# Kernel optimization log

Measured on AMD Instinct MI355X. Metric: run time of the kernel, lower is better.

The kernel has to match this reference:

```python
import jax, jax.numpy as jnp
import numpy as np

B, N, F, H, C, HID = 2, 2048, 64, 4, 32, 128
HIN = H * C  # 128, GAT output width (concat heads)


def setup_inputs() -> dict:
    key = jax.random.key(0)
    ks = jax.random.split(key, 16)
    glorot = jax.nn.initializers.glorot_normal()
    x = jax.random.normal(ks[0], (B, N, F), jnp.float32)
    a = (jax.random.uniform(ks[1], (B, N, N)) < 0.01).astype(jnp.float32)
    a = jnp.maximum(a, jnp.eye(N, dtype=jnp.float32)[None])
    h = jax.random.normal(ks[2], (B, N, HID), jnp.float32)
    # GATConv params (spektral batch mode, concat_heads=True)
    kernel = glorot(ks[3], (F, H, C), jnp.float32)
    attn_self = glorot(ks[4], (H, C), jnp.float32)
    attn_nei = glorot(ks[5], (H, C), jnp.float32)
    bias_gat = jnp.zeros((HIN,), jnp.float32)
    # GRU-style gate params
    b_u = glorot(ks[6], (N, 1), jnp.float32)
    b_r = glorot(ks[7], (N, 1), jnp.float32)
    b_c = glorot(ks[8], (N, 1), jnp.float32)
    W_u = glorot(ks[9], (HID + HIN, HID), jnp.float32)
    W_r = glorot(ks[10], (HID + HIN, HID), jnp.float32)
    W_c = glorot(ks[11], (HID + HIN, HID), jnp.float32)
    # bilinear decoder (p) weight
    R_p = glorot(ks[12], (HID, HID), jnp.float32)
    return {"x": x, "a": a, "h": h, "kernel": kernel, "attn_self": attn_self,
            "attn_nei": attn_nei, "bias_gat": bias_gat, "b_u": b_u, "b_r": b_r,
            "b_c": b_c, "W_u": W_u, "W_r": W_r, "W_c": W_c, "R_p": R_p}


def _gat(x, a, kernel, attn_self, attn_nei, bias_gat):
    # x: [B,N,F] -> per-head features xp: [B,N,H,C]
    xp = jnp.einsum('bnf,fhc->bnhc', x, kernel)
    es = jnp.einsum('bnhc,hc->bnh', xp, attn_self)   # target score
    en = jnp.einsum('bnhc,hc->bnh', xp, attn_nei)    # source score
    # e[b,i,j,h] = leakyrelu(es_i + en_j), masked by adjacency
    e = jax.nn.leaky_relu(es[:, :, None, :] + en[:, None, :, :], 0.2)
    e = e + (-1e9) * (1.0 - a)[..., None]
    alpha = jax.nn.softmax(e, axis=2)                # softmax over sources j
    out = jnp.einsum('bijh,bjhc->bihc', alpha, xp)   # aggregate
    return out.reshape(out.shape[0], out.shape[1], -1) + bias_gat  # [B,N,H*C]


def reference(x, a, h, kernel, attn_self, attn_nei, bias_gat,
              b_u, b_r, b_c, W_u, W_r, W_c, R_p):
    conv_u = _gat(x, a, kernel, attn_self, attn_nei, bias_gat)  # [B,N,HIN]
    z = jnp.concatenate([conv_u, h], axis=-1)                    # [B,N,HIN+HID]
    u = jax.nn.sigmoid(b_u + z @ W_u)                            # b_u [N,1] broadcasts
    r = jax.nn.sigmoid(b_r + z @ W_r)
    zc = jnp.concatenate([conv_u, r * h], axis=-1)
    c = jnp.tanh(b_c + zc @ W_c)
    h_prime = u * h + (1.0 - u) * c                              # [B,N,HID]
    A = jnp.einsum('bnh,hk,bmk->bnm', h_prime, R_p, h_prime)     # bilinear decode [B,N,N]
    return A, h_prime
```

## Files before the change

kernel.cpp:

```cpp
#include <hip/hip_runtime.h>
#include <hip/hip_bf16.h>
#include <math.h>

#define NB 2
#define NN 2048
#define FD 64
#define NH 4
#define HIDD 128
#define ROWS_TOT (NB*NN)

#define XP_OFF   0
#define ES_OFF   524288
#define EN_OFF   540672
#define CU_OFF   557056
#define TBF_OFF  1081344
#define HPBF_OFF 1343488
#define WUH_OFF  1605632
#define WUL_OFF  1622016
#define WRH_OFF  1638400
#define WRL_OFF  1654784
#define WCH_OFF  1671168
#define WCL_OFF  1687552
#define RPH_OFF  1703936
#define RPL_OFF  1712128

#define A_ELEMS (NB*NN*NN)

typedef __attribute__((ext_vector_type(8))) short bf16x8;
typedef __attribute__((ext_vector_type(8))) unsigned short ushort8;
typedef __attribute__((ext_vector_type(4))) unsigned short ushort4v;
typedef __attribute__((ext_vector_type(4))) float f32x4;

#define MFMA_BF16(a,b,c) __builtin_amdgcn_mfma_f32_16x16x32_bf16((a),(b),(c),0,0,0)

static __device__ inline unsigned short f2bf(float x) {
  __hip_bfloat16 b = __float2bfloat16(x);
  unsigned short u; __builtin_memcpy(&u, &b, 2); return u;
}
static __device__ inline float bf2f(unsigned short u) {
  __hip_bfloat16 b; __builtin_memcpy(&b, &u, 2); return __bfloat162float(b);
}
static __device__ inline void split2(float x, unsigned short& hi, unsigned short& lo) {
  hi = f2bf(x);
  lo = f2bf(x - bf2f(hi));
}

__global__ __launch_bounds__(256) void k0_prep(
    const float* __restrict__ Wu, const float* __restrict__ Wr,
    const float* __restrict__ Wc, const float* __restrict__ Rp,
    unsigned short* __restrict__ wuh, unsigned short* __restrict__ wul,
    unsigned short* __restrict__ wrh, unsigned short* __restrict__ wrl,
    unsigned short* __restrict__ wch, unsigned short* __restrict__ wcl,
    unsigned short* __restrict__ rph, unsigned short* __restrict__ rpl)
{
  const int gid = blockIdx.x*256 + threadIdx.x;
  if (gid < 98304) {
    const int which = gid >> 15;
    const int loc = gid & 32767;
    const int j = loc >> 8, k = loc & 255;
    const float* W = which == 0 ? Wu : (which == 1 ? Wr : Wc);
    unsigned short* oh = which == 0 ? wuh : (which == 1 ? wrh : wch);
    unsigned short* ol = which == 0 ? wul : (which == 1 ? wrl : wcl);
    unsigned short h, l; split2(W[k*128 + j], h, l);
    oh[loc] = h; ol[loc] = l;
  } else if (gid < 114688) {
    const int loc = gid - 98304;
    const int j = loc >> 7, k = loc & 127;
    unsigned short h, l; split2(Rp[k*128 + j], h, l);
    rph[loc] = h; rpl[loc] = l;
  }
}

__global__ __launch_bounds__(256) void k1_xp(
    const float* __restrict__ x, const float* __restrict__ kern,
    const float* __restrict__ as_, const float* __restrict__ an_,
    float* __restrict__ xp, float* __restrict__ es, float* __restrict__ en)
{
  __shared__ float xr[8][FD];
  const int t = threadIdx.x;
  const int row0 = blockIdx.x * 8;
  for (int idx = t; idx < 8*FD; idx += 256)
    xr[idx >> 6][idx & 63] = x[(size_t)row0*FD + idx];
  __syncthreads();
  const int c4 = (t & 31) * 4;
  const int rq = t >> 5;
  const float4 asv = *(const float4*)(as_ + c4);
  const float4 anv = *(const float4*)(an_ + c4);
  float4 acc = make_float4(0.f, 0.f, 0.f, 0.f);
  for (int f = 0; f < FD; ++f) {
    const float4 kv = *(const float4*)(kern + f*128 + c4);
    const float xv = xr[rq][f];
    acc.x = fmaf(xv, kv.x, acc.x);
    acc.y = fmaf(xv, kv.y, acc.y);
    acc.z = fmaf(xv, kv.z, acc.z);
    acc.w = fmaf(xv, kv.w, acc.w);
  }
  const int grow = row0 + rq;
  *(float4*)(xp + (size_t)grow*128 + c4) = acc;
  float s  = acc.x*asv.x + acc.y*asv.y + acc.z*asv.z + acc.w*asv.w;
  float n_ = acc.x*anv.x + acc.y*anv.y + acc.z*anv.z + acc.w*anv.w;
#pragma unroll
  for (int mk = 4; mk >= 1; mk >>= 1) {
    s  += __shfl_xor(s,  mk, 64);
    n_ += __shfl_xor(n_, mk, 64);
  }
  if ((t & 7) == 0) {
    const int h = (t & 31) >> 3;
    es[grow*NH + h] = s; en[grow*NH + h] = n_;
  }
}

__global__ __launch_bounds__(256) void k2_attn(
    const float* __restrict__ a, const float* __restrict__ xp,
    const float* __restrict__ es, const float* __restrict__ en,
    const float* __restrict__ bias, float* __restrict__ cu)
{
  __shared__ unsigned short sidx[4][NN];
  __shared__ float swl[4][64][NH];
  const int t = threadIdx.x;
  const int ln = t & 63, wv = t >> 6;
  const int row = blockIdx.x * 4 + wv;
  const int b = row >> 11;
  const float4 esi = *(const float4*)(es + (size_t)row*NH);

  int deg = 0;
  const float4* arow4 = (const float4*)(a + (size_t)row*NN);
#pragma unroll
  for (int cch = 0; cch < 8; ++cch) {
    const float4 v = arow4[cch*64 + ln];
    const int j0 = cch*256 + ln*4;
    const float vv[4] = {v.x, v.y, v.z, v.w};
#pragma unroll
    for (int q = 0; q < 4; ++q) {
      const unsigned long long m = __ballot(vv[q] > 0.5f);
      if (vv[q] > 0.5f) {
        const int pos = deg + (int)__popcll(m & ((1ull << ln) - 1ull));
        sidx[wv][pos] = (unsigned short)(j0 + q);
      }
      deg += (int)__popcll(m);
    }
  }

  const int col0 = ln, col1 = ln + 64;
  const int h0 = ln >> 5;
  float m0=-1e30f, m1=-1e30f, m2=-1e30f, m3=-1e30f;
  float s0=0.f, s1=0.f, s2=0.f, s3=0.f;
  float acc0=0.f, acc1=0.f;
  for (int base = 0; base < deg; base += 64) {
    const int rem = min(64, deg - base);
    float t0=-1e30f, t1=-1e30f, t2=-1e30f, t3=-1e30f;
    if (ln < rem) {
      const int j = sidx[wv][base + ln];
      const float4 e4 = *(const float4*)(en + (size_t)(b*NN + j)*NH);
      t0 = esi.x + e4.x; t0 = t0 > 0.f ? t0 : 0.2f*t0;
      t1 = esi.y + e4.y; t1 = t1 > 0.f ? t1 : 0.2f*t1;
      t2 = esi.z + e4.z; t2 = t2 > 0.f ? t2 : 0.2f*t2;
      t3 = esi.w + e4.w; t3 = t3 > 0.f ? t3 : 0.2f*t3;
    }
    float c0=t0, c1=t1, c2=t2, c3=t3;
#pragma unroll
    for (int mk = 32; mk >= 1; mk >>= 1) {
      c0 = fmaxf(c0, __shfl_xor(c0, mk));
      c1 = fmaxf(c1, __shfl_xor(c1, mk));
      c2 = fmaxf(c2, __shfl_xor(c2, mk));
      c3 = fmaxf(c3, __shfl_xor(c3, mk));
    }
    const float nm0 = fmaxf(m0,c0), nm1 = fmaxf(m1,c1);
    const float nm2 = fmaxf(m2,c2), nm3 = fmaxf(m3,c3);
    const float r0 = expf(m0-nm0), r1 = expf(m1-nm1);
    const float r2 = expf(m2-nm2), r3 = expf(m3-nm3);
    s0 *= r0; s1 *= r1; s2 *= r2; s3 *= r3;
    float w0=0.f, w1=0.f, w2=0.f, w3=0.f;
    if (ln < rem) {
      w0 = expf(t0-nm0); w1 = expf(t1-nm1);
      w2 = expf(t2-nm2); w3 = expf(t3-nm3);
    }
    float u0=w0, u1=w1, u2=w2, u3=w3;
#pragma unroll
    for (int mk = 32; mk >= 1; mk >>= 1) {
      u0 += __shfl_xor(u0, mk);
      u1 += __shfl_xor(u1, mk);
      u2 += __shfl_xor(u2, mk);
      u3 += __shfl_xor(u3, mk);
    }
    s0 += u0; s1 += u1; s2 += u2; s3 += u3;
    acc0 *= (h0 ? r1 : r0);
    acc1 *= (h0 ? r3 : r2);
    swl[wv][ln][0] = w0; swl[wv][ln][1] = w1;
    swl[wv][ln][2] = w2; swl[wv][ln][3] = w3;
#pragma unroll 4
    for (int k = 0; k < rem; ++k) {
      const int j = sidx[wv][base + k];
      const float* xr = xp + (size_t)(b*NN + j)*128;
      acc0 = fmaf(swl[wv][k][h0],     xr[col0], acc0);
      acc1 = fmaf(swl[wv][k][2 + h0], xr[col1], acc1);
    }
    m0=nm0; m1=nm1; m2=nm2; m3=nm3;
  }
  const float den0 = h0 ? s1 : s0;
  const float den1 = h0 ? s3 : s2;
  cu[(size_t)row*128 + col0] = acc0/den0 + bias[col0];
  cu[(size_t)row*128 + col1] = acc1/den1 + bias[col1];
}

__global__ __launch_bounds__(256) void k3_mfma(
    const float* __restrict__ cu_, const float* __restrict__ hin,
    const float* __restrict__ bu, const float* __restrict__ br,
    const float* __restrict__ bc,
    const unsigned short* __restrict__ wuh, const unsigned short* __restrict__ wul,
    const unsigned short* __restrict__ wrh, const unsigned short* __restrict__ wrl,
    const unsigned short* __restrict__ wch, const unsigned short* __restrict__ wcl,
    const unsigned short* __restrict__ rph, const unsigned short* __restrict__ rpl,
    float* __restrict__ hp_out,
    __hip_bfloat16* __restrict__ hp_bf, __hip_bfloat16* __restrict__ t_bf)
{
  __shared__ __align__(16) char zH[16*512];
  __shared__ __align__(16) char zL[16*512];
  __shared__ __align__(16) char rhH[16*256];
  __shared__ __align__(16) char rhL[16*256];
  __shared__ __align__(16) char hpH[16*256];
  __shared__ __align__(16) char hpLo[16*256];
  const int t = threadIdx.x;
  const int row0 = blockIdx.x * 16;

#pragma unroll
  for (int i = 0; i < 4; ++i) {
    const int q = t + 256*i;
    const int r = q >> 6;
    const int c = (q & 63) * 4;
    float4 v;
    if (c < 128) v = *(const float4*)(cu_ + (size_t)(row0+r)*128 + c);
    else         v = *(const float4*)(hin + (size_t)(row0+r)*128 + (c-128));
    unsigned short hx, lx, hy, ly, hz, lz, hw, lw;
    split2(v.x, hx, lx); split2(v.y, hy, ly);
    split2(v.z, hz, lz); split2(v.w, hw, lw);
    ushort4v h4; h4[0]=hx; h4[1]=hy; h4[2]=hz; h4[3]=hw;
    ushort4v l4; l4[0]=lx; l4[1]=ly; l4[2]=lz; l4[3]=lw;
    const int byte = (c*2) ^ ((r & 7) << 4);
    *(ushort4v*)(zH + r*512 + byte) = h4;
    *(ushort4v*)(zL + r*512 + byte) = l4;
  }
  __syncthreads();

  const int ln = t & 63, wv = t >> 6;
  const int n0 = wv * 32;
  const int lr = ln & 15, kid = ln >> 4;
  const int sw = (lr & 7) << 4;
  const f32x4 zero = {0.f, 0.f, 0.f, 0.f};

  f32x4 accU[2] = {zero, zero}, accR[2] = {zero, zero};
#pragma unroll
  for (int ks = 0; ks < 8; ++ks) {
    const int kb = ks*64 + kid*16;
    const bf16x8 ah = *(const bf16x8*)(zH + lr*512 + (kb ^ sw));
    const bf16x8 al = *(const bf16x8*)(zL + lr*512 + (kb ^ sw));
#pragma unroll
    for (int nt = 0; nt < 2; ++nt) {
      const int j = n0 + nt*16 + lr;
      const bf16x8 buH = *(const bf16x8*)((const char*)wuh + j*512 + kb);
      const bf16x8 buL = *(const bf16x8*)((const char*)wul + j*512 + kb);
      const bf16x8 brH = *(const bf16x8*)((const char*)wrh + j*512 + kb);
      const bf16x8 brL = *(const bf16x8*)((const char*)wrl + j*512 + kb);
      accU[nt] = MFMA_BF16(ah, buH, accU[nt]);
      accU[nt] = MFMA_BF16(ah, buL, accU[nt]);
      accU[nt] = MFMA_BF16(al, buH, accU[nt]);
      accR[nt] = MFMA_BF16(ah, brH, accR[nt]);
      accR[nt] = MFMA_BF16(ah, brL, accR[nt]);
      accR[nt] = MFMA_BF16(al, brH, accR[nt]);
    }
  }

  float hval[2][4], uval[2][4];
#pragma unroll
  for (int nt = 0; nt < 2; ++nt) {
    const int colg = n0 + nt*16 + lr;
#pragma unroll
    for (int reg = 0; reg < 4; ++reg) {
      const int row16 = kid*4 + reg;
      const int grow = row0 + row16;
      const int nrow = grow & (NN-1);
      const float h_ = hin[(size_t)grow*128 + colg];
      const float uv = 1.f/(1.f + expf(-(bu[nrow] + accU[nt][reg])));
      const float rv = 1.f/(1.f + expf(-(br[nrow] + accR[nt][reg])));
      hval[nt][reg] = h_; uval[nt][reg] = uv;
      unsigned short hs, ls; split2(rv * h_, hs, ls);
      const int byte = (colg*2) ^ ((row16 & 7) << 4);
      *(unsigned short*)(rhH + row16*256 + byte) = hs;
      *(unsigned short*)(rhL + row16*256 + byte) = ls;
    }
  }
  __syncthreads();

  f32x4 accC[2] = {zero, zero};
#pragma unroll
  for (int ks = 0; ks < 8; ++ks) {
    const int kb = ks*64 + kid*16;
    bf16x8 ah, al;
    if (ks < 4) {
      ah = *(const bf16x8*)(zH + lr*512 + (kb ^ sw));
      al = *(const bf16x8*)(zL + lr*512 + (kb ^ sw));
    } else {
      const int kb2 = (ks-4)*64 + kid*16;
      ah = *(const bf16x8*)(rhH + lr*256 + (kb2 ^ sw));
      al = *(const bf16x8*)(rhL + lr*256 + (kb2 ^ sw));
    }
#pragma unroll
    for (int nt = 0; nt < 2; ++nt) {
      const int j = n0 + nt*16 + lr;
      const bf16x8 bH = *(const bf16x8*)((const char*)wch + j*512 + kb);
      const bf16x8 bL = *(const bf16x8*)((const char*)wcl + j*512 + kb);
      accC[nt] = MFMA_BF16(ah, bH, accC[nt]);
      accC[nt] = MFMA_BF16(ah, bL, accC[nt]);
      accC[nt] = MFMA_BF16(al, bH, accC[nt]);
    }
  }

#pragma unroll
  for (int nt = 0; nt < 2; ++nt) {
    const int colg = n0 + nt*16 + lr;
#pragma unroll
    for (int reg = 0; reg < 4; ++reg) {
      const int row16 = kid*4 + reg;
      const int grow = row0 + row16;
      const int nrow = grow & (NN-1);
      const float cc = tanhf(bc[nrow] + accC[nt][reg]);
      const float uv = uval[nt][reg];
      const float hpv = uv*hval[nt][reg] + (1.f - uv)*cc;
      hp_out[(size_t)grow*128 + colg] = hpv;
      hp_bf[(size_t)grow*128 + colg] = __float2bfloat16(hpv);
      unsigned short hs, ls; split2(hpv, hs, ls);
      const int byte = (colg*2) ^ ((row16 & 7) << 4);
      *(unsigned short*)(hpH  + row16*256 + byte) = hs;
      *(unsigned short*)(hpLo + row16*256 + byte) = ls;
    }
  }
  __syncthreads();

  f32x4 accT[2] = {zero, zero};
#pragma unroll
  for (int ks = 0; ks < 4; ++ks) {
    const int kb = ks*64 + kid*16;
    const bf16x8 ah = *(const bf16x8*)(hpH  + lr*256 + (kb ^ sw));
    const bf16x8 al = *(const bf16x8*)(hpLo + lr*256 + (kb ^ sw));
#pragma unroll
    for (int nt = 0; nt < 2; ++nt) {
      const int j = n0 + nt*16 + lr;
      const bf16x8 bH = *(const bf16x8*)((const char*)rph + j*256 + kb);
      const bf16x8 bL = *(const bf16x8*)((const char*)rpl + j*256 + kb);
      accT[nt] = MFMA_BF16(ah, bH, accT[nt]);
      accT[nt] = MFMA_BF16(ah, bL, accT[nt]);
      accT[nt] = MFMA_BF16(al, bH, accT[nt]);
    }
  }
#pragma unroll
  for (int nt = 0; nt < 2; ++nt) {
    const int colg = n0 + nt*16 + lr;
#pragma unroll
    for (int reg = 0; reg < 4; ++reg) {
      const int grow = row0 + kid*4 + reg;
      t_bf[(size_t)grow*128 + colg] = __float2bfloat16(accT[nt][reg]);
    }
  }
}

__global__ __launch_bounds__(256) void k4b_dec(
    const __hip_bfloat16* __restrict__ t_bf,
    const __hip_bfloat16* __restrict__ hp_bf,
    float* __restrict__ A)
{
  __shared__ __align__(16) char Alds[128*256];
  __shared__ __align__(16) char Blds[128*256];
  const int t = threadIdx.x;
  const int ln = t & 63, wv = t >> 6;
  const int b = blockIdx.z;
  const int i0 = blockIdx.y * 128, j0 = blockIdx.x * 128;

  {
    const int sub = ln >> 4;
    const int cb  = (ln & 15) * 16;
#pragma unroll
    for (int q = 0; q < 8; ++q) {
      const int chunk = wv*8 + q;
      const int row = chunk*4 + sub;
      const int scb = cb ^ ((row & 7) << 4);
      const ushort8 va = *(const ushort8*)
          ((const char*)(t_bf + ((size_t)(b*NN) + i0 + row)*128) + cb);
      *(ushort8*)(Alds + row*256 + scb) = va;
      const ushort8 vb = *(const ushort8*)
          ((const char*)(hp_bf + ((size_t)(b*NN) + j0 + row)*128) + cb);
      *(ushort8*)(Blds + row*256 + scb) = vb;
    }
  }
  __syncthreads();

  const int wr = wv >> 1, wc = wv & 1;
  const int lrow = ln & 15;
  const int kid  = ln >> 4;
  f32x4 acc[4][4];
  const f32x4 zero = {0.f, 0.f, 0.f, 0.f};
#pragma unroll
  for (int m = 0; m < 4; ++m)
#pragma unroll
    for (int n = 0; n < 4; ++n) acc[m][n] = zero;

#pragma unroll
  for (int ks = 0; ks < 4; ++ks) {
    const int kb = ks*64 + kid*16;
    bf16x8 af[4], bfr[4];
#pragma unroll
    for (int m = 0; m < 4; ++m) {
      const int arow = wr*64 + m*16 + lrow;
      af[m] = *(const bf16x8*)(Alds + arow*256 + (kb ^ ((arow & 7) << 4)));
      const int brow = wc*64 + m*16 + lrow;
      bfr[m] = *(const bf16x8*)(Blds + brow*256 + (kb ^ ((brow & 7) << 4)));
    }
#pragma unroll
    for (int m = 0; m < 4; ++m)
#pragma unroll
      for (int n = 0; n < 4; ++n)
        acc[m][n] = MFMA_BF16(af[m], bfr[n], acc[m][n]);
  }

#pragma unroll
  for (int m = 0; m < 4; ++m) {
    const int grow = i0 + wr*64 + m*16 + (ln >> 4)*4;
#pragma unroll
    for (int n = 0; n < 4; ++n) {
      const int gcol = j0 + wc*64 + n*16 + (ln & 15);
      float* Ap = A + ((size_t)b*NN + grow)*NN + gcol;
#pragma unroll
      for (int r = 0; r < 4; ++r)
        Ap[(size_t)r*NN] = acc[m][n][r];
    }
  }
}

extern "C" void kernel_launch(void* const* d_in, const int* in_sizes, int n_in,
                              void* d_out, int out_size, void* d_ws, size_t ws_size,
                              hipStream_t stream)
{
  const float* x    = (const float*)d_in[0];
  const float* a    = (const float*)d_in[1];
  const float* h    = (const float*)d_in[2];
  const float* kern = (const float*)d_in[3];
  const float* as_  = (const float*)d_in[4];
  const float* an_  = (const float*)d_in[5];
  const float* bias = (const float*)d_in[6];
  const float* bu   = (const float*)d_in[7];
  const float* br   = (const float*)d_in[8];
  const float* bc   = (const float*)d_in[9];
  const float* Wu   = (const float*)d_in[10];
  const float* Wr   = (const float*)d_in[11];
  const float* Wc   = (const float*)d_in[12];
  const float* Rp   = (const float*)d_in[13];
  (void)in_sizes; (void)n_in; (void)out_size; (void)ws_size;

  float* ws = (float*)d_ws;
  float* xp = ws + XP_OFF;
  float* es = ws + ES_OFF;
  float* en = ws + EN_OFF;
  float* cu = ws + CU_OFF;
  __hip_bfloat16* t_bf  = (__hip_bfloat16*)(ws + TBF_OFF);
  __hip_bfloat16* hp_bf = (__hip_bfloat16*)(ws + HPBF_OFF);
  unsigned short* wuh = (unsigned short*)(ws + WUH_OFF);
  unsigned short* wul = (unsigned short*)(ws + WUL_OFF);
  unsigned short* wrh = (unsigned short*)(ws + WRH_OFF);
  unsigned short* wrl = (unsigned short*)(ws + WRL_OFF);
  unsigned short* wch = (unsigned short*)(ws + WCH_OFF);
  unsigned short* wcl = (unsigned short*)(ws + WCL_OFF);
  unsigned short* rph = (unsigned short*)(ws + RPH_OFF);
  unsigned short* rpl = (unsigned short*)(ws + RPL_OFF);

  float* A  = (float*)d_out;
  float* hp = (float*)d_out + A_ELEMS;

  hipLaunchKernelGGL(k0_prep, dim3(448), dim3(256), 0, stream,
                     Wu, Wr, Wc, Rp, wuh, wul, wrh, wrl, wch, wcl, rph, rpl);
  hipLaunchKernelGGL(k1_xp,   dim3(ROWS_TOT/8), dim3(256), 0, stream,
                     x, kern, as_, an_, xp, es, en);
  hipLaunchKernelGGL(k2_attn, dim3(ROWS_TOT/4), dim3(256), 0, stream,
                     a, xp, es, en, bias, cu);
  hipLaunchKernelGGL(k3_mfma, dim3(ROWS_TOT/16), dim3(256), 0, stream,
                     cu, h, bu, br, bc, wuh, wul, wrh, wrl, wch, wcl, rph, rpl,
                     hp, hp_bf, t_bf);
  hipLaunchKernelGGL(k4b_dec, dim3(NN/128, NN/128, NB), dim3(256), 0, stream,
                     t_bf, hp_bf, A);
}
```

Baseline: 153.3 us.

## Pre-swizzle weights into MFMA fragment order, widen GRU block, stage decoder output

The prep kernel now stores split bf16 weights in per-lane MFMA fragment order, so the gate kernel reads B operands as fully coalesced 16-byte vectors. The gate kernel is widened to 512 threads, with each wave owning one 16-column tile instead of two. The decoder kernel stages its 128x128 fp32 tile through padded LDS (reusing the A/B buffers) and writes rows as coalesced float4, replacing scattered 4-byte stores. This costs an extra LDS round trip and two barriers in the decoder, plus more LDS per block, which may reduce occupancy.

```diff
diff --git a/kernel.cpp b/kernel.cpp
--- a/kernel.cpp
+++ b/kernel.cpp
@@ -57,7 +57,12 @@
   if (gid < 98304) {
     const int which = gid >> 15;
     const int loc = gid & 32767;
-    const int j = loc >> 8, k = loc & 255;
+    const int e  = loc & 7;
+    const int ln = (loc >> 3) & 63;
+    const int ks = (loc >> 9) & 7;
+    const int jt = loc >> 12;
+    const int j = jt*16 + (ln & 15);
+    const int k = ks*32 + ((ln >> 4) << 3) + e;
     const float* W = which == 0 ? Wu : (which == 1 ? Wr : Wc);
     unsigned short* oh = which == 0 ? wuh : (which == 1 ? wrh : wch);
     unsigned short* ol = which == 0 ? wul : (which == 1 ? wrl : wcl);
@@ -65,7 +70,12 @@
     oh[loc] = h; ol[loc] = l;
   } else if (gid < 114688) {
     const int loc = gid - 98304;
-    const int j = loc >> 7, k = loc & 127;
+    const int e  = loc & 7;
+    const int ln = (loc >> 3) & 63;
+    const int ks = (loc >> 9) & 3;
+    const int jt = loc >> 11;
+    const int j = jt*16 + (ln & 15);
+    const int k = ks*32 + ((ln >> 4) << 3) + e;
     unsigned short h, l; split2(Rp[k*128 + j], h, l);
     rph[loc] = h; rpl[loc] = l;
   }
@@ -203,7 +213,7 @@
   cu[(size_t)row*128 + col1] = acc1/den1 + bias[col1];
 }
 
-__global__ __launch_bounds__(256) void k3_mfma(
+__global__ __launch_bounds__(512) void k3_mfma(
     const float* __restrict__ cu_, const float* __restrict__ hin,
     const float* __restrict__ bu, const float* __restrict__ br,
     const float* __restrict__ bc,
@@ -224,8 +234,8 @@
   const int row0 = blockIdx.x * 16;
 
 #pragma unroll
-  for (int i = 0; i < 4; ++i) {
-    const int q = t + 256*i;
+  for (int i = 0; i < 2; ++i) {
+    const int q = t + 512*i;
     const int r = q >> 6;
     const int c = (q & 63) * 4;
     float4 v;
@@ -243,55 +253,56 @@
   __syncthreads();
 
   const int ln = t & 63, wv = t >> 6;
-  const int n0 = wv * 32;
   const int lr = ln & 15, kid = ln >> 4;
   const int sw = (lr & 7) << 4;
+  const int colg = wv*16 + lr;
   const f32x4 zero = {0.f, 0.f, 0.f, 0.f};
-
-  f32x4 accU[2] = {zero, zero}, accR[2] = {zero, zero};
+  const bf16x8* wuhF = (const bf16x8*)wuh;
+  const bf16x8* wulF = (const bf16x8*)wul;
+  const bf16x8* wrhF = (const bf16x8*)wrh;
+  const bf16x8* wrlF = (const bf16x8*)wrl;
+  const bf16x8* wchF = (const bf16x8*)wch;
+  const bf16x8* wclF = (const bf16x8*)wcl;
+  const bf16x8* rphF = (const bf16x8*)rph;
+  const bf16x8* rplF = (const bf16x8*)rpl;
+
+  f32x4 accU = zero, accR = zero;
 #pragma unroll
   for (int ks = 0; ks < 8; ++ks) {
     const int kb = ks*64 + kid*16;
     const bf16x8 ah = *(const bf16x8*)(zH + lr*512 + (kb ^ sw));
     const bf16x8 al = *(const bf16x8*)(zL + lr*512 + (kb ^ sw));
-#pragma unroll
-    for (int nt = 0; nt < 2; ++nt) {
-      const int j = n0 + nt*16 + lr;
-      const bf16x8 buH = *(const bf16x8*)((const char*)wuh + j*512 + kb);
-      const bf16x8 buL = *(const bf16x8*)((const char*)wul + j*512 + kb);
-      const bf16x8 brH = *(const bf16x8*)((const char*)wrh + j*512 + kb);
-      const bf16x8 brL = *(const bf16x8*)((const char*)wrl + j*512 + kb);
-      accU[nt] = MFMA_BF16(ah, buH, accU[nt]);
-      accU[nt] = MFMA_BF16(ah, buL, accU[nt]);
-      accU[nt] = MFMA_BF16(al, buH, accU[nt]);
-      accR[nt] = MFMA_BF16(ah, brH, accR[nt]);
-      accR[nt] = MFMA_BF16(ah, brL, accR[nt]);
-      accR[nt] = MFMA_BF16(al, brH, accR[nt]);
-    }
-  }
-
-  float hval[2][4], uval[2][4];
-#pragma unroll
-  for (int nt = 0; nt < 2; ++nt) {
-    const int colg = n0 + nt*16 + lr;
-#pragma unroll
-    for (int reg = 0; reg < 4; ++reg) {
-      const int row16 = kid*4 + reg;
-      const int grow = row0 + row16;
-      const int nrow = grow & (NN-1);
-      const float h_ = hin[(size_t)grow*128 + colg];
-      const float uv = 1.f/(1.f + expf(-(bu[nrow] + accU[nt][reg])));
-      const float rv = 1.f/(1.f + expf(-(br[nrow] + accR[nt][reg])));
-      hval[nt][reg] = h_; uval[nt][reg] = uv;
-      unsigned short hs, ls; split2(rv * h_, hs, ls);
-      const int byte = (colg*2) ^ ((row16 & 7) << 4);
-      *(unsigned short*)(rhH + row16*256 + byte) = hs;
-      *(unsigned short*)(rhL + row16*256 + byte) = ls;
-    }
-  }
-  __syncthreads();
-
-  f32x4 accC[2] = {zero, zero};
+    const int fb = (wv*8 + ks)*64 + ln;
+    const bf16x8 buH = wuhF[fb];
+    const bf16x8 buL = wulF[fb];
+    const bf16x8 brH = wrhF[fb];
+    const bf16x8 brL = wrlF[fb];
+    accU = MFMA_BF16(ah, buH, accU);
+    accU = MFMA_BF16(ah, buL, accU);
+    accU = MFMA_BF16(al, buH, accU);
+    accR = MFMA_BF16(ah, brH, accR);
+    accR = MFMA_BF16(ah, brL, accR);
+    accR = MFMA_BF16(al, brH, accR);
+  }
+
+  float hval[4], uval[4];
+#pragma unroll
+  for (int reg = 0; reg < 4; ++reg) {
+    const int row16 = kid*4 + reg;
+    const int grow = row0 + row16;
+    const int nrow = grow & (NN-1);
+    const float h_ = hin[(size_t)grow*128 + colg];
+    const float uv = 1.f/(1.f + expf(-(bu[nrow] + accU[reg])));
+    const float rv = 1.f/(1.f + expf(-(br[nrow] + accR[reg])));
+    hval[reg] = h_; uval[reg] = uv;
+    unsigned short hs, ls; split2(rv * h_, hs, ls);
+    const int byte = (colg*2) ^ ((row16 & 7) << 4);
+    *(unsigned short*)(rhH + row16*256 + byte) = hs;
+    *(unsigned short*)(rhL + row16*256 + byte) = ls;
+  }
+  __syncthreads();
+
+  f32x4 accC = zero;
 #pragma unroll
   for (int ks = 0; ks < 8; ++ks) {
     const int kb = ks*64 + kid*16;
@@ -304,62 +315,48 @@
       ah = *(const bf16x8*)(rhH + lr*256 + (kb2 ^ sw));
       al = *(const bf16x8*)(rhL + lr*256 + (kb2 ^ sw));
     }
-#pragma unroll
-    for (int nt = 0; nt < 2; ++nt) {
-      const int j = n0 + nt*16 + lr;
-      const bf16x8 bH = *(const bf16x8*)((const char*)wch + j*512 + kb);
-      const bf16x8 bL = *(const bf16x8*)((const char*)wcl + j*512 + kb);
-      accC[nt] = MFMA_BF16(ah, bH, accC[nt]);
-      accC[nt] = MFMA_BF16(ah, bL, accC[nt]);
-      accC[nt] = MFMA_BF16(al, bH, accC[nt]);
-    }
-  }
-
-#pragma unroll
-  for (int nt = 0; nt < 2; ++nt) {
-    const int colg = n0 + nt*16 + lr;
-#pragma unroll
-    for (int reg = 0; reg < 4; ++reg) {
-      const int row16 = kid*4 + reg;
-      const int grow = row0 + row16;
-      const int nrow = grow & (NN-1);
-      const float cc = tanhf(bc[nrow] + accC[nt][reg]);
-      const float uv = uval[nt][reg];
-      const float hpv = uv*hval[nt][reg] + (1.f - uv)*cc;
-      hp_out[(size_t)grow*128 + colg] = hpv;
-      hp_bf[(size_t)grow*128 + colg] = __float2bfloat16(hpv);
-      unsigned short hs, ls; split2(hpv, hs, ls);
-      const int byte = (colg*2) ^ ((row16 & 7) << 4);
-      *(unsigned short*)(hpH  + row16*256 + byte) = hs;
-      *(unsigned short*)(hpLo + row16*256 + byte) = ls;
-    }
-  }
-  __syncthreads();
-
-  f32x4 accT[2] = {zero, zero};
+    const int fb = (wv*8 + ks)*64 + ln;
+    const bf16x8 bH = wchF[fb];
+    const bf16x8 bL = wclF[fb];
+    accC = MFMA_BF16(ah, bH, accC);
+    accC = MFMA_BF16(ah, bL, accC);
+    accC = MFMA_BF16(al, bH, accC);
+  }
+
+#pragma unroll
+  for (int reg = 0; reg < 4; ++reg) {
+    const int row16 = kid*4 + reg;
+    const int grow = row0 + row16;
+    const int nrow = grow & (NN-1);
+    const float cc = tanhf(bc[nrow] + accC[reg]);
+    const float uv = uval[reg];
+    const float hpv = uv*hval[reg] + (1.f - uv)*cc;
+    hp_out[(size_t)grow*128 + colg] = hpv;
+    hp_bf[(size_t)grow*128 + colg] = __float2bfloat16(hpv);
+    unsigned short hs, ls; split2(hpv, hs, ls);
+    const int byte = (colg*2) ^ ((row16 & 7) << 4);
+    *(unsigned short*)(hpH  + row16*256 + byte) = hs;
+    *(unsigned short*)(hpLo + row16*256 + byte) = ls;
+  }
+  __syncthreads();
+
+  f32x4 accT = zero;
 #pragma unroll
   for (int ks = 0; ks < 4; ++ks) {
     const int kb = ks*64 + kid*16;
     const bf16x8 ah = *(const bf16x8*)(hpH  + lr*256 + (kb ^ sw));
     const bf16x8 al = *(const bf16x8*)(hpLo + lr*256 + (kb ^ sw));
-#pragma unroll
-    for (int nt = 0; nt < 2; ++nt) {
-      const int j = n0 + nt*16 + lr;
-      const bf16x8 bH = *(const bf16x8*)((const char*)rph + j*256 + kb);
-      const bf16x8 bL = *(const bf16x8*)((const char*)rpl + j*256 + kb);
-      accT[nt] = MFMA_BF16(ah, bH, accT[nt]);
-      accT[nt] = MFMA_BF16(ah, bL, accT[nt]);
-      accT[nt] = MFMA_BF16(al, bH, accT[nt]);
-    }
-  }
-#pragma unroll
-  for (int nt = 0; nt < 2; ++nt) {
-    const int colg = n0 + nt*16 + lr;
-#pragma unroll
-    for (int reg = 0; reg < 4; ++reg) {
-      const int grow = row0 + kid*4 + reg;
-      t_bf[(size_t)grow*128 + colg] = __float2bfloat16(accT[nt][reg]);
-    }
+    const int fb = (wv*4 + ks)*64 + ln;
+    const bf16x8 bH = rphF[fb];
+    const bf16x8 bL = rplF[fb];
+    accT = MFMA_BF16(ah, bH, accT);
+    accT = MFMA_BF16(ah, bL, accT);
+    accT = MFMA_BF16(al, bH, accT);
+  }
+#pragma unroll
+  for (int reg = 0; reg < 4; ++reg) {
+    const int grow = row0 + kid*4 + reg;
+    t_bf[(size_t)grow*128 + colg] = __float2bfloat16(accT[reg]);
   }
 }
 
@@ -368,8 +365,10 @@
     const __hip_bfloat16* __restrict__ hp_bf,
     float* __restrict__ A)
 {
-  __shared__ __align__(16) char Alds[128*256];
-  __shared__ __align__(16) char Blds[128*256];
+  __shared__ __align__(16) char smem[128*132*4];
+  char* Alds = smem;
+  char* Blds = smem + 32768;
+  float* Cst = (float*)smem;
   const int t = threadIdx.x;
   const int ln = t & 63, wv = t >> 6;
   const int b = blockIdx.z;
@@ -420,18 +419,27 @@
       for (int n = 0; n < 4; ++n)
         acc[m][n] = MFMA_BF16(af[m], bfr[n], acc[m][n]);
   }
+  __syncthreads();
 
 #pragma unroll
   for (int m = 0; m < 4; ++m) {
-    const int grow = i0 + wr*64 + m*16 + (ln >> 4)*4;
+    const int crow = wr*64 + m*16 + kid*4;
 #pragma unroll
     for (int n = 0; n < 4; ++n) {
-      const int gcol = j0 + wc*64 + n*16 + (ln & 15);
-      float* Ap = A + ((size_t)b*NN + grow)*NN + gcol;
+      const int ccol = wc*64 + n*16 + lrow;
 #pragma unroll
       for (int r = 0; r < 4; ++r)
-        Ap[(size_t)r*NN] = acc[m][n][r];
-    }
+        Cst[(crow + r)*132 + ccol] = acc[m][n][r];
+    }
+  }
+  __syncthreads();
+
+#pragma unroll
+  for (int p = 0; p < 16; ++p) {
+    const int row = p*8 + (t >> 5);
+    const int c4  = (t & 31) * 4;
+    const float4 v = *(const float4*)&Cst[row*132 + c4];
+    *(float4*)(A + ((size_t)b*NN + i0 + row)*NN + j0 + c4) = v;
   }
 }
 
@@ -480,7 +488,7 @@
                      x, kern, as_, an_, xp, es, en);
   hipLaunchKernelGGL(k2_attn, dim3(ROWS_TOT/4), dim3(256), 0, stream,
                      a, xp, es, en, bias, cu);
-  hipLaunchKernelGGL(k3_mfma, dim3(ROWS_TOT/16), dim3(256), 0, stream,
+  hipLaunchKernelGGL(k3_mfma, dim3(ROWS_TOT/16), dim3(512), 0, stream,
                      cu, h, bu, br, bc, wuh, wul, wrh, wrl, wch, wcl, rph, rpl,
                      hp, hp_bf, t_bf);
   hipLaunchKernelGGL(k4b_dec, dim3(NN/128, NN/128, NB), dim3(256), 0, stream,
```

Measured after the change: 143.5 us. 1.07x faster.
